# Optimization experiments

Measured on AMD Instinct MI355X. Metric: run time of the kernel, lower is better.

The kernel has to match this reference:

```python
import jax, jax.numpy as jnp
import numpy as np

EPS = 1e-8  # torch.nn.CosineSimilarity default eps


def setup_inputs() -> dict:
    key = jax.random.key(0)
    k1, k2 = jax.random.split(key)
    action_set = jax.random.normal(k1, (1_000_000, 64), dtype=jnp.float32)
    pred_action = jax.random.normal(k2, (32, 4, 64), dtype=jnp.float32)
    return {"pred_action": pred_action, "action_set": action_set}


def reference(pred_action, action_set):
    # pred_action: [B, T, D] (a 2-D [B, D] input would be unsqueezed to T=1)
    # action_set:  [N, D]
    if pred_action.ndim == 2:
        pred_action = pred_action[:, None, :]
    # torch CosineSimilarity: x1.x2 / max(||x1|| * ||x2||, eps)
    dot = jnp.einsum('nd,btd->nbt', action_set, pred_action)        # [N, B, T]
    na = jnp.linalg.norm(action_set, axis=-1)                       # [N]
    nb = jnp.linalg.norm(pred_action, axis=-1)                      # [B, T]
    sims = dot / jnp.maximum(na[:, None, None] * nb[None, :, :], EPS)
    amax = jnp.argmax(sims, axis=0)                                  # [B, T]
    return action_set[amax]                                          # [B, T, D]
```

## Files before the change

kernel.cpp:

```cpp
#include <hip/hip_runtime.h>
#include <hip/hip_bf16.h>
#include <math.h>

#define D        64
#define NQ       128
#define TS       64
#define ASTRIDE  72
#define MARGIN   0.025f
#define MAXTILES 15648
#define CAP      128

typedef __attribute__((ext_vector_type(8))) short  short8;
typedef __attribute__((ext_vector_type(4))) short  short4v;
typedef __attribute__((ext_vector_type(4))) float  f32x4;

__device__ inline unsigned ordf(float f) {
    unsigned u = __float_as_uint(f);
    return (u & 0x80000000u) ? ~u : (u | 0x80000000u);
}

__device__ inline short bf16bits(float f) {
    __hip_bfloat16 h = __float2bfloat16(f);
    return *(short*)&h;
}

__device__ inline short8 cvt8(f32x4 a, f32x4 b, float s) {
    short8 r;
    r[0] = bf16bits(a.x * s); r[1] = bf16bits(a.y * s);
    r[2] = bf16bits(a.z * s); r[3] = bf16bits(a.w * s);
    r[4] = bf16bits(b.x * s); r[5] = bf16bits(b.y * s);
    r[6] = bf16bits(b.z * s); r[7] = bf16bits(b.w * s);
    return r;
}

__global__ __launch_bounds__(256, 2)
void k1_score(const float* __restrict__ pred,
              const float* __restrict__ acts,
              float* __restrict__ tmax,
              int ntiles)
{
    __shared__ unsigned short As[TS * ASTRIDE];
    __shared__ float rna[TS];

    const int tid  = threadIdx.x;
    const int lane = tid & 63;
    const int wv   = tid >> 6;
    const int quad = lane >> 4;
    const int l15  = lane & 15;

    short8 bfrag[2][2];
#pragma unroll
    for (int nt = 0; nt < 2; ++nt) {
        const int q = wv * 32 + nt * 16 + l15;
        const float* P = pred + q * D + quad * 8;
        f32x4 v0 = *(const f32x4*)(P);
        f32x4 v1 = *(const f32x4*)(P + 4);
        f32x4 v2 = *(const f32x4*)(P + 32);
        f32x4 v3 = *(const f32x4*)(P + 36);
        float nb2 = v0.x*v0.x + v0.y*v0.y + v0.z*v0.z + v0.w*v0.w
                  + v1.x*v1.x + v1.y*v1.y + v1.z*v1.z + v1.w*v1.w
                  + v2.x*v2.x + v2.y*v2.y + v2.z*v2.z + v2.w*v2.w
                  + v3.x*v3.x + v3.y*v3.y + v3.z*v3.z + v3.w*v3.w;
        nb2 += __shfl_xor(nb2, 16);
        nb2 += __shfl_xor(nb2, 32);
        const float rnb = 1.0f / sqrtf(nb2);
        bfrag[nt][0] = cvt8(v0, v1, rnb);
        bfrag[nt][1] = cvt8(v2, v3, rnb);
    }

    for (int tile = blockIdx.x; tile < ntiles; tile += gridDim.x) {
        const f32x4* src = (const f32x4*)(acts + (size_t)tile * (TS * D));
#pragma unroll
        for (int i = 0; i < 4; ++i) {
            int c  = tid + i * 256;
            int r  = c >> 4;
            int c4 = c & 15;
            f32x4 v = src[c];
            float s = v.x*v.x + v.y*v.y + v.z*v.z + v.w*v.w;
            s += __shfl_xor(s, 1); s += __shfl_xor(s, 2);
            s += __shfl_xor(s, 4); s += __shfl_xor(s, 8);
            if ((tid & 15) == 0) rna[r] = 1.0f / sqrtf(s);
            short4v b;
            b[0] = bf16bits(v.x); b[1] = bf16bits(v.y);
            b[2] = bf16bits(v.z); b[3] = bf16bits(v.w);
            *(short4v*)&As[r * ASTRIDE + c4 * 4] = b;
        }
        __syncthreads();

        f32x4 acc[4][2];
#pragma unroll
        for (int mt = 0; mt < 4; ++mt)
#pragma unroll
            for (int nt = 0; nt < 2; ++nt)
                acc[mt][nt] = (f32x4){0.f, 0.f, 0.f, 0.f};

#pragma unroll
        for (int mt = 0; mt < 4; ++mt) {
            const int row = mt * 16 + l15;
            short8 a0 = *(const short8*)&As[row * ASTRIDE + quad * 8];
            short8 a1 = *(const short8*)&As[row * ASTRIDE + 32 + quad * 8];
#pragma unroll
            for (int nt = 0; nt < 2; ++nt) {
                acc[mt][nt] = __builtin_amdgcn_mfma_f32_16x16x32_bf16(a0, bfrag[nt][0], acc[mt][nt], 0, 0, 0);
                acc[mt][nt] = __builtin_amdgcn_mfma_f32_16x16x32_bf16(a1, bfrag[nt][1], acc[mt][nt], 0, 0, 0);
            }
        }

        float m0 = -3.0e38f, m1 = -3.0e38f;
#pragma unroll
        for (int mt = 0; mt < 4; ++mt) {
            f32x4 r4 = *(const f32x4*)&rna[mt * 16 + quad * 4];
            m0 = fmaxf(m0, acc[mt][0].x * r4.x); m1 = fmaxf(m1, acc[mt][1].x * r4.x);
            m0 = fmaxf(m0, acc[mt][0].y * r4.y); m1 = fmaxf(m1, acc[mt][1].y * r4.y);
            m0 = fmaxf(m0, acc[mt][0].z * r4.z); m1 = fmaxf(m1, acc[mt][1].z * r4.z);
            m0 = fmaxf(m0, acc[mt][0].w * r4.w); m1 = fmaxf(m1, acc[mt][1].w * r4.w);
        }
        m0 = fmaxf(m0, __shfl_xor(m0, 16)); m0 = fmaxf(m0, __shfl_xor(m0, 32));
        m1 = fmaxf(m1, __shfl_xor(m1, 16)); m1 = fmaxf(m1, __shfl_xor(m1, 32));
        if (lane < 32) {
            int nt = lane >> 4;
            tmax[(size_t)tile * NQ + wv * 32 + nt * 16 + (lane & 15)] = nt ? m1 : m0;
        }
        __syncthreads();
    }
}

__global__ __launch_bounds__(256, 1)
void k2_rescore(const float* __restrict__ pred,
                const float* __restrict__ acts,
                const float* __restrict__ tmax,
                float* __restrict__ out,
                int ntiles)
{
    __shared__ float col[MAXTILES];
    __shared__ float wmax[4];
    __shared__ int   cnt;
    __shared__ int   list[CAP];

    const int q   = blockIdx.x;
    const int tid = threadIdx.x;

    float m = -3.0e38f;
    for (int t = tid; t < ntiles; t += 256) {
        float v = tmax[(size_t)t * NQ + q];
        col[t] = v;
        m = fmaxf(m, v);
    }
#pragma unroll
    for (int off = 1; off < 64; off <<= 1)
        m = fmaxf(m, __shfl_xor(m, off));
    if ((tid & 63) == 0) wmax[tid >> 6] = m;
    if (tid == 0) cnt = 0;
    __syncthreads();
    m = fmaxf(fmaxf(wmax[0], wmax[1]), fmaxf(wmax[2], wmax[3]));
    const float thr = m - MARGIN;

    for (int t = tid; t < ntiles; t += 256) {
        if (col[t] >= thr) {
            int i = atomicAdd(&cnt, 1);
            if (i < CAP) list[i] = t;
        }
    }
    __syncthreads();
    const int n = min(cnt, CAP);

    if (tid < 64) {
        const f32x4* P = (const f32x4*)(pred + q * D);
        unsigned long long best = 0ull;
        for (int i = 0; i < n; ++i) {
            const int row = list[i] * TS + tid;
            const f32x4* A = (const f32x4*)(acts + (size_t)row * D);
            float dot = 0.f, na2 = 0.f;
#pragma unroll
            for (int c = 0; c < 16; ++c) {
                f32x4 a = A[c];
                f32x4 p = P[c];
                dot = fmaf(a.x, p.x, dot); na2 = fmaf(a.x, a.x, na2);
                dot = fmaf(a.y, p.y, dot); na2 = fmaf(a.y, a.y, na2);
                dot = fmaf(a.z, p.z, dot); na2 = fmaf(a.z, a.z, na2);
                dot = fmaf(a.w, p.w, dot); na2 = fmaf(a.w, a.w, na2);
            }
            float sim = dot * (1.0f / sqrtf(na2));
            unsigned long long key =
                ((unsigned long long)ordf(sim) << 32) | (unsigned)(~row);
#pragma unroll
            for (int off = 1; off < 64; off <<= 1) {
                unsigned long long o = __shfl_xor(key, off);
                if (o > key) key = o;
            }
            if (key > best) best = key;
        }
        const unsigned idx = ~(unsigned)(best & 0xffffffffull);
        out[q * D + tid] = acts[(size_t)idx * D + tid];
    }
}

extern "C" void kernel_launch(void* const* d_in, const int* in_sizes, int n_in,
                              void* d_out, int out_size, void* d_ws, size_t ws_size,
                              hipStream_t stream)
{
    const float* pred = (const float*)d_in[0];
    const float* acts = (const float*)d_in[1];
    long n0 = in_sizes[0], n1 = in_sizes[1];
    if (n0 > n1) {
        const float* t = pred; pred = acts; acts = t;
        long tt = n0; n0 = n1; n1 = tt;
    }
    const int N      = (int)(n1 / D);
    const int ntiles = N / TS;

    float* tmax = (float*)d_ws;
    float* out  = (float*)d_out;

    k1_score<<<dim3(1024), dim3(256), 0, stream>>>(pred, acts, tmax, ntiles);
    k2_rescore<<<dim3(NQ), dim3(256), 0, stream>>>(pred, acts, tmax, out, ntiles);
}
```

Before: 386.3 us.

## Give each wave its own action tile, loading fragments directly without LDS

The scoring kernel now assigns a whole 64-row action tile to each wavefront. The wavefront loads the fp32 rows straight into MFMA fragment registers, normalizes them in registers, and runs all 128 queries against them, so the shared-memory staging and block barriers are gone. The tile-max buffer is transposed to query-major so the rescore kernel reads each query's row contiguously, and the large LDS column cache in that kernel is dropped, allowing two blocks per CU. The grid shrinks to 512 blocks, and the higher register use from holding all query fragments may reduce occupancy.

```diff
diff --git a/kernel.cpp b/kernel.cpp
--- a/kernel.cpp
+++ b/kernel.cpp
@@ -5,13 +5,10 @@
 #define D        64
 #define NQ       128
 #define TS       64
-#define ASTRIDE  72
 #define MARGIN   0.025f
-#define MAXTILES 15648
 #define CAP      128
 
 typedef __attribute__((ext_vector_type(8))) short  short8;
-typedef __attribute__((ext_vector_type(4))) short  short4v;
 typedef __attribute__((ext_vector_type(4))) float  f32x4;
 
 __device__ inline unsigned ordf(float f) {
@@ -22,6 +19,15 @@
 __device__ inline short bf16bits(float f) {
     __hip_bfloat16 h = __float2bfloat16(f);
     return *(short*)&h;
+}
+
+__device__ inline float sq16(f32x4 a, f32x4 b, f32x4 c, f32x4 d) {
+    float s = 0.f;
+    s = fmaf(a.x, a.x, s); s = fmaf(a.y, a.y, s); s = fmaf(a.z, a.z, s); s = fmaf(a.w, a.w, s);
+    s = fmaf(b.x, b.x, s); s = fmaf(b.y, b.y, s); s = fmaf(b.z, b.z, s); s = fmaf(b.w, b.w, s);
+    s = fmaf(c.x, c.x, s); s = fmaf(c.y, c.y, s); s = fmaf(c.z, c.z, s); s = fmaf(c.w, c.w, s);
+    s = fmaf(d.x, d.x, s); s = fmaf(d.y, d.y, s); s = fmaf(d.z, d.z, s); s = fmaf(d.w, d.w, s);
+    return s;
 }
 
 __device__ inline short8 cvt8(f32x4 a, f32x4 b, float s) {
@@ -39,124 +45,108 @@
               float* __restrict__ tmax,
               int ntiles)
 {
-    __shared__ unsigned short As[TS * ASTRIDE];
-    __shared__ float rna[TS];
-
     const int tid  = threadIdx.x;
     const int lane = tid & 63;
-    const int wv   = tid >> 6;
     const int quad = lane >> 4;
     const int l15  = lane & 15;
-
-    short8 bfrag[2][2];
-#pragma unroll
-    for (int nt = 0; nt < 2; ++nt) {
-        const int q = wv * 32 + nt * 16 + l15;
+    const int wid  = blockIdx.x * 4 + (tid >> 6);
+    const int nw   = gridDim.x * 4;
+
+    short8 bf[8][2];
+#pragma unroll
+    for (int nt = 0; nt < 8; ++nt) {
+        const int q = nt * 16 + l15;
         const float* P = pred + q * D + quad * 8;
         f32x4 v0 = *(const f32x4*)(P);
         f32x4 v1 = *(const f32x4*)(P + 4);
         f32x4 v2 = *(const f32x4*)(P + 32);
         f32x4 v3 = *(const f32x4*)(P + 36);
-        float nb2 = v0.x*v0.x + v0.y*v0.y + v0.z*v0.z + v0.w*v0.w
-                  + v1.x*v1.x + v1.y*v1.y + v1.z*v1.z + v1.w*v1.w
-                  + v2.x*v2.x + v2.y*v2.y + v2.z*v2.z + v2.w*v2.w
-                  + v3.x*v3.x + v3.y*v3.y + v3.z*v3.z + v3.w*v3.w;
+        float nb2 = sq16(v0, v1, v2, v3);
         nb2 += __shfl_xor(nb2, 16);
         nb2 += __shfl_xor(nb2, 32);
         const float rnb = 1.0f / sqrtf(nb2);
-        bfrag[nt][0] = cvt8(v0, v1, rnb);
-        bfrag[nt][1] = cvt8(v2, v3, rnb);
-    }
-
-    for (int tile = blockIdx.x; tile < ntiles; tile += gridDim.x) {
-        const f32x4* src = (const f32x4*)(acts + (size_t)tile * (TS * D));
-#pragma unroll
-        for (int i = 0; i < 4; ++i) {
-            int c  = tid + i * 256;
-            int r  = c >> 4;
-            int c4 = c & 15;
-            f32x4 v = src[c];
-            float s = v.x*v.x + v.y*v.y + v.z*v.z + v.w*v.w;
-            s += __shfl_xor(s, 1); s += __shfl_xor(s, 2);
-            s += __shfl_xor(s, 4); s += __shfl_xor(s, 8);
-            if ((tid & 15) == 0) rna[r] = 1.0f / sqrtf(s);
-            short4v b;
-            b[0] = bf16bits(v.x); b[1] = bf16bits(v.y);
-            b[2] = bf16bits(v.z); b[3] = bf16bits(v.w);
-            *(short4v*)&As[r * ASTRIDE + c4 * 4] = b;
-        }
-        __syncthreads();
-
-        f32x4 acc[4][2];
-#pragma unroll
-        for (int mt = 0; mt < 4; ++mt)
-#pragma unroll
-            for (int nt = 0; nt < 2; ++nt)
-                acc[mt][nt] = (f32x4){0.f, 0.f, 0.f, 0.f};
-
+        bf[nt][0] = cvt8(v0, v1, rnb);
+        bf[nt][1] = cvt8(v2, v3, rnb);
+    }
+
+    for (int tile = wid; tile < ntiles; tile += nw) {
+        const float* base = acts + (size_t)tile * (TS * D);
+
+        f32x4 af[4][2][2];
 #pragma unroll
         for (int mt = 0; mt < 4; ++mt) {
-            const int row = mt * 16 + l15;
-            short8 a0 = *(const short8*)&As[row * ASTRIDE + quad * 8];
-            short8 a1 = *(const short8*)&As[row * ASTRIDE + 32 + quad * 8];
-#pragma unroll
-            for (int nt = 0; nt < 2; ++nt) {
-                acc[mt][nt] = __builtin_amdgcn_mfma_f32_16x16x32_bf16(a0, bfrag[nt][0], acc[mt][nt], 0, 0, 0);
-                acc[mt][nt] = __builtin_amdgcn_mfma_f32_16x16x32_bf16(a1, bfrag[nt][1], acc[mt][nt], 0, 0, 0);
-            }
-        }
-
-        float m0 = -3.0e38f, m1 = -3.0e38f;
+            const float* rp = base + (mt * 16 + l15) * D + quad * 8;
+#pragma unroll
+            for (int ks = 0; ks < 2; ++ks) {
+                af[mt][ks][0] = *(const f32x4*)(rp + ks * 32);
+                af[mt][ks][1] = *(const f32x4*)(rp + ks * 32 + 4);
+            }
+        }
+
+        short8 abf[4][2];
 #pragma unroll
         for (int mt = 0; mt < 4; ++mt) {
-            f32x4 r4 = *(const f32x4*)&rna[mt * 16 + quad * 4];
-            m0 = fmaxf(m0, acc[mt][0].x * r4.x); m1 = fmaxf(m1, acc[mt][1].x * r4.x);
-            m0 = fmaxf(m0, acc[mt][0].y * r4.y); m1 = fmaxf(m1, acc[mt][1].y * r4.y);
-            m0 = fmaxf(m0, acc[mt][0].z * r4.z); m1 = fmaxf(m1, acc[mt][1].z * r4.z);
-            m0 = fmaxf(m0, acc[mt][0].w * r4.w); m1 = fmaxf(m1, acc[mt][1].w * r4.w);
-        }
-        m0 = fmaxf(m0, __shfl_xor(m0, 16)); m0 = fmaxf(m0, __shfl_xor(m0, 32));
-        m1 = fmaxf(m1, __shfl_xor(m1, 16)); m1 = fmaxf(m1, __shfl_xor(m1, 32));
-        if (lane < 32) {
-            int nt = lane >> 4;
-            tmax[(size_t)tile * NQ + wv * 32 + nt * 16 + (lane & 15)] = nt ? m1 : m0;
-        }
-        __syncthreads();
-    }
-}
-
-__global__ __launch_bounds__(256, 1)
+            float s = sq16(af[mt][0][0], af[mt][0][1], af[mt][1][0], af[mt][1][1]);
+            s += __shfl_xor(s, 16);
+            s += __shfl_xor(s, 32);
+            const float r = 1.0f / sqrtf(s);
+            abf[mt][0] = cvt8(af[mt][0][0], af[mt][0][1], r);
+            abf[mt][1] = cvt8(af[mt][1][0], af[mt][1][1], r);
+        }
+
+#pragma unroll
+        for (int nt = 0; nt < 8; ++nt) {
+            f32x4 acc[4];
+#pragma unroll
+            for (int mt = 0; mt < 4; ++mt) acc[mt] = (f32x4){0.f, 0.f, 0.f, 0.f};
+#pragma unroll
+            for (int ks = 0; ks < 2; ++ks)
+#pragma unroll
+                for (int mt = 0; mt < 4; ++mt)
+                    acc[mt] = __builtin_amdgcn_mfma_f32_16x16x32_bf16(
+                        abf[mt][ks], bf[nt][ks], acc[mt], 0, 0, 0);
+
+            float m = -3.0e38f;
+#pragma unroll
+            for (int mt = 0; mt < 4; ++mt) {
+                m = fmaxf(m, fmaxf(fmaxf(acc[mt].x, acc[mt].y),
+                                   fmaxf(acc[mt].z, acc[mt].w)));
+            }
+            m = fmaxf(m, __shfl_xor(m, 16));
+            m = fmaxf(m, __shfl_xor(m, 32));
+            if (quad == 0)
+                tmax[(size_t)(nt * 16 + l15) * ntiles + tile] = m;
+        }
+    }
+}
+
+__global__ __launch_bounds__(256, 2)
 void k2_rescore(const float* __restrict__ pred,
                 const float* __restrict__ acts,
                 const float* __restrict__ tmax,
                 float* __restrict__ out,
                 int ntiles)
 {
-    __shared__ float col[MAXTILES];
     __shared__ float wmax[4];
     __shared__ int   cnt;
     __shared__ int   list[CAP];
 
     const int q   = blockIdx.x;
     const int tid = threadIdx.x;
-
+    const float* row = tmax + (size_t)q * ntiles;
+
+    if (tid == 0) cnt = 0;
     float m = -3.0e38f;
-    for (int t = tid; t < ntiles; t += 256) {
-        float v = tmax[(size_t)t * NQ + q];
-        col[t] = v;
-        m = fmaxf(m, v);
-    }
-#pragma unroll
-    for (int off = 1; off < 64; off <<= 1)
-        m = fmaxf(m, __shfl_xor(m, off));
+    for (int t = tid; t < ntiles; t += 256) m = fmaxf(m, row[t]);
+#pragma unroll
+    for (int off = 1; off < 64; off <<= 1) m = fmaxf(m, __shfl_xor(m, off));
     if ((tid & 63) == 0) wmax[tid >> 6] = m;
-    if (tid == 0) cnt = 0;
     __syncthreads();
     m = fmaxf(fmaxf(wmax[0], wmax[1]), fmaxf(wmax[2], wmax[3]));
     const float thr = m - MARGIN;
 
     for (int t = tid; t < ntiles; t += 256) {
-        if (col[t] >= thr) {
+        if (row[t] >= thr) {
             int i = atomicAdd(&cnt, 1);
             if (i < CAP) list[i] = t;
         }
@@ -168,8 +158,8 @@
         const f32x4* P = (const f32x4*)(pred + q * D);
         unsigned long long best = 0ull;
         for (int i = 0; i < n; ++i) {
-            const int row = list[i] * TS + tid;
-            const f32x4* A = (const f32x4*)(acts + (size_t)row * D);
+            const int r = list[i] * TS + tid;
+            const f32x4* A = (const f32x4*)(acts + (size_t)r * D);
             float dot = 0.f, na2 = 0.f;
 #pragma unroll
             for (int c = 0; c < 16; ++c) {
@@ -182,7 +172,7 @@
             }
             float sim = dot * (1.0f / sqrtf(na2));
             unsigned long long key =
-                ((unsigned long long)ordf(sim) << 32) | (unsigned)(~row);
+                ((unsigned long long)ordf(sim) << 32) | (unsigned)(~r);
 #pragma unroll
             for (int off = 1; off < 64; off <<= 1) {
                 unsigned long long o = __shfl_xor(key, off);
@@ -212,6 +202,6 @@
     float* tmax = (float*)d_ws;
     float* out  = (float*)d_out;
 
-    k1_score<<<dim3(1024), dim3(256), 0, stream>>>(pred, acts, tmax, ntiles);
+    k1_score<<<dim3(512), dim3(256), 0, stream>>>(pred, acts, tmax, ntiles);
     k2_rescore<<<dim3(NQ), dim3(256), 0, stream>>>(pred, acts, tmax, out, ntiles);
 }
```

Result: no change. 392.8 us (+1.7%).
